# Kernel tuning notes

Hardware: AMD Instinct MI355X
Metric: run time of the kernel (lower is better)

The kernel has to match this reference:

```python
import jax, jax.numpy as jnp
import numpy as np
import math

G_GRAPHS = 32   # graphs per batch
NPG = 2048      # nodes per graph
DEG = 8         # avg degree
IN_DIM = 128
HID = 128

def _lin(k, fi, fo):
    return jax.random.normal(k, (fi, fo), jnp.float32) / np.sqrt(fi).astype(np.float32)

def setup_inputs():
    key = jax.random.key(0)
    ks = jax.random.split(key, 32)
    Nt = G_GRAPHS * NPG
    Epg = NPG * DEG
    E = G_GRAPHS * Epg
    x = jax.random.normal(ks[0], (Nt, IN_DIM), jnp.float32)
    src = jax.random.randint(ks[1], (E,), 0, NPG)
    dst = jax.random.randint(ks[2], (E,), 0, NPG)
    off = (jnp.arange(E) // Epg) * NPG  # keep edges within their graph block
    edge_index = jnp.stack([src + off, dst + off]).astype(jnp.int32)
    batch = (jnp.arange(Nt) // NPG).astype(jnp.int32)
    p = {}
    dims = [(IN_DIM, HID), (HID, HID), (HID, HID), (HID, HID)]
    for i, (fi, fo) in enumerate(dims, 1):
        p['Wl%d' % i] = _lin(ks[3 * i], fi, fo)
        p['bl%d' % i] = jnp.zeros((fo,), jnp.float32)
        p['Wr%d' % i] = _lin(ks[3 * i + 1], fi, fo)
    for j in (1, 2):  # SAGPooling score GNN (GraphConv hidden->1)
        p['Prel%d' % j] = _lin(ks[15 + 2 * j], HID, 1)
        p['prb%d' % j] = jnp.zeros((1,), jnp.float32)
        p['Proot%d' % j] = _lin(ks[16 + 2 * j], HID, 1)
    p['W5'] = _lin(ks[24], HID, 64); p['b5'] = jnp.zeros((64,), jnp.float32)
    p['W6'] = _lin(ks[25], 64, 2);  p['b6'] = jnp.zeros((2,), jnp.float32)
    return dict(x=x, edge_index=edge_index, batch=batch, npg=NPG, **p)

def reference(x, edge_index, batch, npg,
              Wl1, bl1, Wr1, Wl2, bl2, Wr2, Wl3, bl3, Wr3, Wl4, bl4, Wr4,
              Prel1, prb1, Proot1, Prel2, prb2, Proot2, W5, b5, W6, b6):
    src, dst = edge_index[0], edge_index[1]
    Nt = x.shape[0]
    Gn = Nt // npg

    def sage(h, em, Wl, bl, Wr):
        # SAGEConv (mean aggr): lin_l(mean_j x_j) + lin_r(x_root)
        s = jax.ops.segment_sum(h[src] * em[:, None], dst, num_segments=Nt)
        c = jax.ops.segment_sum(em, dst, num_segments=Nt)
        return (s / jnp.maximum(c, 1.0)[:, None]) @ Wl + bl + h @ Wr

    def pool(h, em, nm, k, Prel, prb, Proot):
        # SAGPooling: score = GraphConv(h) (add aggr), top-k per graph, x *= tanh(score)
        s = jax.ops.segment_sum(h[src] * em[:, None], dst, num_segments=Nt)
        score = (s @ Prel + h @ Proot + prb)[:, 0]
        smr = jnp.where(nm > 0, score, -1e30).reshape(Gn, npg)
        _, idx = jax.lax.top_k(smr, k)
        newm = jnp.zeros((Gn, npg), h.dtype).at[jnp.arange(Gn)[:, None], idx].set(1.0).reshape(-1)
        h = h * jnp.tanh(score)[:, None] * newm[:, None]
        em = em * newm[src] * newm[dst]  # filter_adj: keep edges with both ends kept
        return h, em, newm

    em = jnp.ones(src.shape, x.dtype)
    nm = jnp.ones((Nt,), x.dtype)
    h = jax.nn.relu(sage(x, em, Wl1, bl1, Wr1))
    h = jax.nn.relu(sage(h, em, Wl2, bl2, Wr2))
    k1 = math.ceil(0.5 * npg)
    h, em, nm = pool(h, em, nm, k1, Prel1, prb1, Proot1)
    h = jax.nn.relu(sage(h, em, Wl3, bl3, Wr3)) * nm[:, None]
    h = jax.nn.relu(sage(h, em, Wl4, bl4, Wr4)) * nm[:, None]
    k2 = math.ceil(0.5 * k1)
    h, em, nm = pool(h, em, nm, k2, Prel2, prb2, Proot2)
    # global mean pool over surviving nodes
    sums = jax.ops.segment_sum(h, batch, num_segments=Gn)
    cnt = jax.ops.segment_sum(nm, batch, num_segments=Gn)
    g = sums / jnp.maximum(cnt, 1.0)[:, None]
    g = jax.nn.relu(g @ W5 + b5)
    return jax.nn.log_softmax(g @ W6 + b6, axis=1)
```

## Files before the change

kernel.cpp:

```cpp
#include <hip/hip_runtime.h>
#include <hip/hip_bf16.h>
#include <math.h>

#define NT   65536
#define NPGC 2048
#define NG   32
#define NE   524288
#define EPG  16384
#define HID  128
#define K1   1024
#define K2   512

typedef short short8 __attribute__((ext_vector_type(8)));
typedef float f32x4  __attribute__((ext_vector_type(4)));

__device__ __forceinline__ float bf2f(unsigned short u) {
    union { unsigned int i; float f; } v; v.i = ((unsigned int)u) << 16; return v.f;
}
__device__ __forceinline__ unsigned short f2bf(float f) {
    union { float f; unsigned int i; } v; v.f = f;
    unsigned int x = v.i;
    return (unsigned short)((x + 0x7fffu + ((x >> 16) & 1u)) >> 16);
}
__device__ __forceinline__ void split2(float v, unsigned short& hi, unsigned short& lo) {
    unsigned int b = __float_as_uint(v);
    hi = (unsigned short)(b >> 16);
    float rem = v - __uint_as_float(b & 0xFFFF0000u);
    lo = (unsigned short)(__float_as_uint(rem) >> 16);
}

__global__ void k_detect(const unsigned short* __restrict__ x, int* __restrict__ flag) {
    __shared__ int cnt;
    if (threadIdx.x == 0) cnt = 0;
    __syncthreads();
    int sane = 0;
#pragma unroll
    for (int j = 0; j < 16; ++j) {
        unsigned short u = x[threadIdx.x * 16 + j];
        int e = (u >> 7) & 0xFF;
        if (e > 0x60 && e < 0xA0) sane++;
    }
    atomicAdd(&cnt, sane);
    __syncthreads();
    if (threadIdx.x == 0) *flag = (cnt > 3686) ? 1 : 0;
}

struct CvtDesc { const void* src[22]; int n[22]; int off[22]; };

__global__ void k_cvt(CvtDesc d, float* __restrict__ wts, const int* __restrict__ flag) {
    int t = blockIdx.y;
    int n = d.n[t];
    bool isbf = (*flag != 0);
    const unsigned short* sb = (const unsigned short*)d.src[t];
    const float* sf = (const float*)d.src[t];
    float* o = wts + d.off[t];
    for (int i = blockIdx.x * blockDim.x + threadIdx.x; i < n; i += gridDim.x * blockDim.x)
        o[i] = isbf ? bf2f(sb[i]) : sf[i];
}

__global__ void k_packW(const float* __restrict__ wts, int4 oWl, int4 oWr,
                        unsigned short* __restrict__ Wpack,
                        int* __restrict__ rowc, int* __restrict__ fill) {
    int idx = blockIdx.x * 256 + threadIdx.x;
    if (idx < NT) { rowc[idx] = 0; fill[idx] = 0; }
    if (idx >= 4 * 8 * 8 * 64 * 8) return;
    int L    = idx >> 15;
    int rem  = idx & 32767;
    int ct   = rem >> 12;
    int rem2 = rem & 4095;
    int ks   = rem2 >> 9;
    int rem3 = rem2 & 511;
    int lane = rem3 >> 3;
    int j    = rem3 & 7;
    int k   = ks * 32 + (lane >> 4) * 8 + j;
    int col = ct * 16 + (lane & 15);
    int ol = (L == 0) ? oWl.x : (L == 1) ? oWl.y : (L == 2) ? oWl.z : oWl.w;
    int orr = (L == 0) ? oWr.x : (L == 1) ? oWr.y : (L == 2) ? oWr.z : oWr.w;
    float w = (k < 128) ? wts[ol + k * 128 + col] : wts[orr + (k - 128) * 128 + col];
    unsigned short hi = f2bf(w);
    unsigned short lo = f2bf(w - bf2f(hi));
    int base = L * 65536 + (ct * 8 + ks) * 512 + lane * 8 + j;
    Wpack[base]         = hi;
    Wpack[base + 32768] = lo;
}

__global__ void k_hist(const int* __restrict__ dstE, int* __restrict__ rowc) {
    int e = blockIdx.x * 256 + threadIdx.x;
    if (e < NE) atomicAdd(&rowc[dstE[e]], 1);
}

__global__ void k_scan1(const int* __restrict__ cnt, int* __restrict__ rp, int* __restrict__ bsum,
                        float* __restrict__ invc) {
    __shared__ int s[256];
    int t = threadIdx.x;
    int i = blockIdx.x * 256 + t;
    int v = cnt[i];
    invc[i] = 1.0f / fmaxf((float)v, 1.0f);
    s[t] = v;
    __syncthreads();
    for (int off = 1; off < 256; off <<= 1) {
        int a = (t >= off) ? s[t - off] : 0;
        __syncthreads();
        s[t] += a;
        __syncthreads();
    }
    rp[i] = s[t] - v;
    if (t == 255) bsum[blockIdx.x] = s[255];
}

__global__ void k_scan23(int* __restrict__ rp, const int* __restrict__ bsum) {
    __shared__ int s[256];
    int t = threadIdx.x;
    s[t] = bsum[t];
    __syncthreads();
    for (int off = 1; off < 256; off <<= 1) {
        int a = (t >= off) ? s[t - off] : 0;
        __syncthreads();
        s[t] += a;
        __syncthreads();
    }
    int boffv = s[blockIdx.x] - bsum[blockIdx.x];
    int i = blockIdx.x * 256 + t;
    rp[i] += boffv;
    if (i == 0) rp[NT] = NE;
}

__global__ void k_scatter(const int* __restrict__ src, const int* __restrict__ dst,
                          const int* __restrict__ rp, int* __restrict__ fill, int* __restrict__ col) {
    int e = blockIdx.x * blockDim.x + threadIdx.x;
    if (e < NE) {
        int d = dst[e];
        int p = rp[d] + atomicAdd(&fill[d], 1);
        col[p] = src[e];
    }
}

__global__ void __launch_bounds__(256) k_fcsr(const int* __restrict__ act,
                                              const float* __restrict__ nm,
                                              const int* __restrict__ rp,
                                              const int* __restrict__ col,
                                              int2* __restrict__ rp2,
                                              int* __restrict__ col2,
                                              float* __restrict__ invc) {
    __shared__ int wtot[4];
    int g = blockIdx.x, t = threadIdx.x;
    int lane = t & 63, wv = t >> 6;
    int cb = g * K1;
    int ebase = g * EPG;
    int c[4]; int tsum = 0;
    int bg[4], en[4];
#pragma unroll
    for (int j = 0; j < 4; ++j) {
        int ci = t * 4 + j;
        int n = act[cb + ci];
        bg[j] = rp[n]; en[j] = rp[n + 1];
        int cc = 0;
        for (int e = bg[j]; e < en[j]; ++e) cc += (nm[col[e]] > 0.f) ? 1 : 0;
        c[j] = cc; tsum += cc;
        invc[n] = 1.0f / fmaxf((float)cc, 1.0f);
    }
    int pre = tsum;
#pragma unroll
    for (int off = 1; off < 64; off <<= 1) {
        int v = __shfl_up(pre, off, 64);
        pre += (lane >= off) ? v : 0;
    }
    if (lane == 63) wtot[wv] = pre;
    __syncthreads();
    int woff = 0;
#pragma unroll
    for (int w2 = 0; w2 < 4; ++w2) woff += (w2 < wv) ? wtot[w2] : 0;
    int ex = pre - tsum + woff;
#pragma unroll
    for (int j = 0; j < 4; ++j) {
        int ci = t * 4 + j;
        int p = ebase + ex;
        rp2[cb + ci] = make_int2(p, p + c[j]);
        for (int e = bg[j]; e < en[j]; ++e) {
            int s = col[e];
            if (nm[s] > 0.f) col2[p++] = s;
        }
        ex += c[j];
    }
}

__device__ __forceinline__ int lds_sw(int node, int k) {
    int g = k >> 3;
    int go = g ^ (node & 7);
    return node * 128 + go * 8 + (k & 7);
}

template<int MODE>
__device__ __forceinline__ float4 ldrow4(const void* __restrict__ h, int node, int f) {
    if constexpr (MODE == 1) {
        ushort4 v = *((const ushort4*)h + (size_t)node * 32 + (f >> 2));
        float4 o; o.x = bf2f(v.x); o.y = bf2f(v.y); o.z = bf2f(v.z); o.w = bf2f(v.w);
        return o;
    } else {
        return *((const float4*)h + (size_t)node * 32 + (f >> 2));
    }
}

template<bool HAS_TS, bool COMPACT, int MODE>
__device__ __forceinline__ void sage_body(
    const void* __restrict__ h, const float* __restrict__ ts,
    const float* __restrict__ invc,
    const int* __restrict__ rp, const int2* __restrict__ rp2,
    const int* __restrict__ col,
    const unsigned short* __restrict__ Wp,
    unsigned short* Ahi, unsigned short* Alo,
    unsigned short* Bhi, unsigned short* Blo,
    int n0, int cb, const int* __restrict__ actb, int tid, f32x4 acc[2][2])
{
    int lane = tid & 63, w = tid >> 6;
    int lrow = lane & 15, quad = lane >> 4;
    int gnode = tid >> 5;
    int f = (tid & 31) * 4;

    int gns[4], begs[4], ends[4]; float invs[4];
#pragma unroll
    for (int p = 0; p < 4; ++p) gns[p] = COMPACT ? actb[p * 8 + gnode] : n0 + p * 8 + gnode;
#pragma unroll
    for (int p = 0; p < 4; ++p) {
        if (COMPACT) { int2 be = rp2[cb + p * 8 + gnode]; begs[p] = be.x; ends[p] = be.y; }
        else         { begs[p] = rp[gns[p]]; ends[p] = rp[gns[p] + 1]; }
    }
#pragma unroll
    for (int p = 0; p < 4; ++p) invs[p] = invc[gns[p]];

    float4 rootv[4]; float roots[4];
#pragma unroll
    for (int i = 0; i < 4; ++i) {
        int idx = i * 256 + tid;
        int node = idx >> 5;
        int f2 = (idx & 31) * 4;
        int gn = COMPACT ? actb[node] : n0 + node;
        rootv[i] = ldrow4<MODE>(h, gn, f2);
        roots[i] = HAS_TS ? ts[gn] : 1.0f;
    }

#pragma unroll
    for (int pass = 0; pass < 4; ++pass) {
        int node = pass * 8 + gnode;
        float ax = 0.f, ay = 0.f, az = 0.f, aw = 0.f;
        int beg = begs[pass], end = ends[pass];
        int ecl = end - 1;
        for (int e0 = beg; e0 < end; e0 += 8) {
            int sj[8];
#pragma unroll
            for (int j = 0; j < 8; ++j) {
                int e = (e0 + j < end) ? e0 + j : ecl;
                sj[j] = col[e];
            }
            float4 vj[8];
#pragma unroll
            for (int j = 0; j < 8; ++j)
                vj[j] = ldrow4<MODE>(h, sj[j], f);
#pragma unroll
            for (int j = 0; j < 8; ++j) {
                float cj = (e0 + j < end) ? (HAS_TS ? ts[sj[j]] : 1.0f) : 0.0f;
                ax += vj[j].x * cj;
                ay += vj[j].y * cj;
                az += vj[j].z * cj;
                aw += vj[j].w * cj;
            }
        }
        float inv = invs[pass];
        ushort4 hi4, lo4;
        split2(ax * inv, hi4.x, lo4.x);
        split2(ay * inv, hi4.y, lo4.y);
        split2(az * inv, hi4.z, lo4.z);
        split2(aw * inv, hi4.w, lo4.w);
        int a = lds_sw(node, f);
        *(ushort4*)&Ahi[a] = hi4;
        *(ushort4*)&Alo[a] = lo4;
    }

#pragma unroll
    for (int i = 0; i < 4; ++i) {
        int idx = i * 256 + tid;
        int node = idx >> 5;
        int f2 = (idx & 31) * 4;
        float sc = roots[i];
        ushort4 hi4, lo4;
        split2(rootv[i].x * sc, hi4.x, lo4.x);
        split2(rootv[i].y * sc, hi4.y, lo4.y);
        split2(rootv[i].z * sc, hi4.z, lo4.z);
        split2(rootv[i].w * sc, hi4.w, lo4.w);
        int a = lds_sw(node, f2);
        *(ushort4*)&Bhi[a] = hi4;
        *(ushort4*)&Blo[a] = lo4;
    }
    __syncthreads();

#pragma unroll
    for (int ks = 0; ks < 8; ++ks) {
        const unsigned short* Hb = (ks < 4) ? Ahi : Bhi;
        const unsigned short* Lb = (ks < 4) ? Alo : Blo;
        short8 bh[2], blo[2];
#pragma unroll
        for (int c = 0; c < 2; ++c) {
            int ct = 2 * w + c;
            bh[c]  = *(const short8*)&Wp[(ct * 8 + ks) * 512 + lane * 8];
            blo[c] = *(const short8*)&Wp[32768 + (ct * 8 + ks) * 512 + lane * 8];
        }
        int kb = (ks & 3) * 32 + quad * 8;
#pragma unroll
        for (int st = 0; st < 2; ++st) {
            int a = lds_sw(st * 16 + lrow, kb);
            short8 ah = *(const short8*)&Hb[a];
            short8 al = *(const short8*)&Lb[a];
#pragma unroll
            for (int c = 0; c < 2; ++c) {
                acc[st][c] = __builtin_amdgcn_mfma_f32_16x16x32_bf16(ah, bh[c],  acc[st][c], 0, 0, 0);
                acc[st][c] = __builtin_amdgcn_mfma_f32_16x16x32_bf16(al, bh[c],  acc[st][c], 0, 0, 0);
                acc[st][c] = __builtin_amdgcn_mfma_f32_16x16x32_bf16(ah, blo[c], acc[st][c], 0, 0, 0);
            }
        }
    }
}

template<bool COMPACT>
__device__ __forceinline__ void map_block(int b, int& graph, int& tile) {
    if (COMPACT) { graph = (b & 7) * 4 + (b >> 8); tile = (b >> 3) & 31; }
    else         { graph = (b & 7) * 4 + (b >> 9); tile = (b >> 3) & 63; }
}

__global__ void __launch_bounds__(256, 8) k_sage_l1(
    const void* __restrict__ x, const int* __restrict__ flag,
    const float* __restrict__ invc,
    const int* __restrict__ rp, const int* __restrict__ col,
    const unsigned short* __restrict__ Wp, const float* __restrict__ bl,
    float* __restrict__ out)
{
    __shared__ unsigned short Ahi[32 * 128];
    __shared__ unsigned short Alo[32 * 128];
    __shared__ unsigned short Bhi[32 * 128];
    __shared__ unsigned short Blo[32 * 128];
    int tid = threadIdx.x;
    int graph, tile;
    map_block<false>(blockIdx.x, graph, tile);
    int n0 = graph * NPGC + tile * 32;
    int lane = tid & 63, w = tid >> 6;
    int lrow = lane & 15, quad = lane >> 4;
    f32x4 acc[2][2] = {};

    if (*flag)
        sage_body<false, false, 1>(x, nullptr, invc, rp, nullptr, col, Wp, Ahi, Alo, Bhi, Blo, n0, 0, nullptr, tid, acc);
    else
        sage_body<false, false, 0>(x, nullptr, invc, rp, nullptr, col, Wp, Ahi, Alo, Bhi, Blo, n0, 0, nullptr, tid, acc);

#pragma unroll
    for (int c = 0; c < 2; ++c) {
        int colg = (2 * w + c) * 16 + lrow;
        float bias = bl[colg];
#pragma unroll
        for (int st = 0; st < 2; ++st) {
#pragma unroll
            for (int rr = 0; rr < 4; ++rr) {
                int node = n0 + st * 16 + quad * 4 + rr;
                __builtin_nontemporal_store(fmaxf(acc[st][c][rr] + bias, 0.f),
                                            &out[(size_t)node * HID + colg]);
            }
        }
    }
}

__global__ void __launch_bounds__(256, 8) k_sage_plain(
    const float* __restrict__ h, const float* __restrict__ ts,
    const float* __restrict__ invc,
    const int2* __restrict__ rp2, const int* __restrict__ col2,
    const unsigned short* __restrict__ Wp, const float* __restrict__ bl,
    float* __restrict__ out, const int* __restrict__ act)
{
    __shared__ unsigned short Ahi[32 * 128];
    __shared__ unsigned short Alo[32 * 128];
    __shared__ unsigned short Bhi[32 * 128];
    __shared__ unsigned short Blo[32 * 128];
    int tid = threadIdx.x;
    int graph, tile;
    map_block<true>(blockIdx.x, graph, tile);
    int n0 = graph * NPGC + tile * 32;
    int cb = graph * K1 + tile * 32;
    const int* actb = act + cb;
    int lane = tid & 63, w = tid >> 6;
    int lrow = lane & 15, quad = lane >> 4;
    f32x4 acc[2][2] = {};

    sage_body<true, true, 0>(h, ts, invc, nullptr, rp2, col2, Wp, Ahi, Alo, Bhi, Blo, n0, cb, actb, tid, acc);

#pragma unroll
    for (int c = 0; c < 2; ++c) {
        int colg = (2 * w + c) * 16 + lrow;
        float bias = bl[colg];
#pragma unroll
        for (int st = 0; st < 2; ++st) {
#pragma unroll
            for (int rr = 0; rr < 4; ++rr) {
                int node = actb[st * 16 + quad * 4 + rr];
                __builtin_nontemporal_store(fmaxf(acc[st][c][rr] + bias, 0.f),
                                            &out[(size_t)node * HID + colg]);
            }
        }
    }
}

template<bool COMPACT>
__global__ void __launch_bounds__(256, 8) k_sage_dots(
    const float* __restrict__ h,
    const float* __restrict__ invc,
    const int* __restrict__ rp, const int2* __restrict__ rp2,
    const int* __restrict__ col,
    const unsigned short* __restrict__ Wp, const float* __restrict__ bl,
    float* __restrict__ out,
    const float* __restrict__ Prel, const float* __restrict__ Proot,
    float* __restrict__ q, float* __restrict__ r, const int* __restrict__ act)
{
    __shared__ unsigned short Ahi[32 * 128];
    __shared__ unsigned short Alo[32 * 128];
    __shared__ unsigned short Bhi[32 * 128];
    __shared__ unsigned short Blo[32 * 128];
    int tid = threadIdx.x;
    int graph, tile;
    map_block<COMPACT>(blockIdx.x, graph, tile);
    int n0 = graph * NPGC + tile * 32;
    int cb = COMPACT ? (graph * K1 + tile * 32) : 0;
    const int* actb = COMPACT ? (act + cb) : nullptr;
    int lane = tid & 63, w = tid >> 6;
    int lrow = lane & 15, quad = lane >> 4;
    f32x4 acc[2][2] = {};

    sage_body<false, COMPACT, 0>(h, nullptr, invc, rp, rp2, col, Wp, Ahi, Alo, Bhi, Blo, n0, cb, actb, tid, acc);

    float qp[2][4] = {}, rp_[2][4] = {};
#pragma unroll
    for (int c = 0; c < 2; ++c) {
        int colg = (2 * w + c) * 16 + lrow;
        float bias = bl[colg];
        float pq = Prel[colg], pr = Proot[colg];
#pragma unroll
        for (int st = 0; st < 2; ++st) {
#pragma unroll
            for (int rr = 0; rr < 4; ++rr) {
                int nl = st * 16 + quad * 4 + rr;
                int node = COMPACT ? actb[nl] : n0 + nl;
                float val = fmaxf(acc[st][c][rr] + bias, 0.f);
                __builtin_nontemporal_store(val, &out[(size_t)node * HID + colg]);
                qp[st][rr] += val * pq;
                rp_[st][rr] += val * pr;
            }
        }
    }
#pragma unroll
    for (int st = 0; st < 2; ++st)
#pragma unroll
        for (int rr = 0; rr < 4; ++rr) {
#pragma unroll
            for (int m = 1; m < 16; m <<= 1) {
                qp[st][rr]  += __shfl_xor(qp[st][rr],  m, 64);
                rp_[st][rr] += __shfl_xor(rp_[st][rr], m, 64);
            }
        }
    __syncthreads();
    float* qa = (float*)Ahi;
    if (tid < 64) qa[tid] = 0.f;
    __syncthreads();
    if (lrow == 0) {
#pragma unroll
        for (int st = 0; st < 2; ++st)
#pragma unroll
            for (int rr = 0; rr < 4; ++rr) {
                int nl = st * 16 + quad * 4 + rr;
                atomicAdd(&qa[nl], qp[st][rr]);
                atomicAdd(&qa[32 + nl], rp_[st][rr]);
            }
    }
    __syncthreads();
    if (tid < 32) {
        int node = COMPACT ? actb[tid] : n0 + tid;
        q[node] = qa[tid];
        r[node] = qa[32 + tid];
    }
}

__global__ void k_score(const float* __restrict__ q, const float* __restrict__ r,
                        const float* __restrict__ prb,
                        const int* __restrict__ rp, const int* __restrict__ col,
                        float* __restrict__ score) {
    int n = blockIdx.x * 256 + threadIdx.x;
    int beg = rp[n], end = rp[n + 1];
    float s = 0.f;
    for (int e = beg; e < end; ++e) s += q[col[e]];
    score[n] = s + r[n] + prb[0];
}

__global__ void k_score2(const float* __restrict__ q, const float* __restrict__ r,
                         const float* __restrict__ prb,
                         const int2* __restrict__ rp2, const int* __restrict__ col2,
                         float* __restrict__ score, const int* __restrict__ act) {
    int i = blockIdx.x * 256 + threadIdx.x;
    int n = act[i];
    int2 be = rp2[i];
    float s = 0.f;
    for (int e = be.x; e < be.y; ++e) s += q[col2[e]];
    score[n] = s + r[n] + prb[0];
}

template<bool NMIN>
__global__ void __launch_bounds__(256) k_topk(const float* __restrict__ score,
                                              float* __restrict__ nm,
                                              float* __restrict__ tval, int k,
                                              int* __restrict__ act) {
    __shared__ unsigned int u[NPGC];
    __shared__ int hist[256];
    __shared__ int scanb[257];
    __shared__ int wtot[4];
    __shared__ int wtot2[4];
    __shared__ unsigned int s_byte;
    __shared__ int s_kk;
    int tid = threadIdx.x;
    int lane = tid & 63, wv = tid >> 6;
    int base = blockIdx.x * NPGC;

    for (int j = tid; j < NPGC; j += 256) {
        float sc = NMIN ? ((nm[base + j] > 0.f) ? score[base + j] : -1e30f) : score[base + j];
        unsigned int v = __float_as_uint(sc);
        v = (v & 0x80000000u) ? ~v : (v | 0x80000000u);
        u[j] = v;
    }
    hist[tid] = 0;
    if (tid == 0) scanb[256] = 0;
    __syncthreads();

    unsigned int prefix = 0;
    int kk = k;
#pragma unroll
    for (int round = 0; round < 4; ++round) {
        int shift = 24 - 8 * round;
        unsigned int pmask = (round == 0) ? 0u : (0xFFFFFFFFu << (32 - 8 * round));
        for (int j = tid; j < NPGC; j += 256) {
            unsigned int v = u[j];
            if ((v & pmask) == prefix) atomicAdd(&hist[(v >> shift) & 0xFF], 1);
        }
        __syncthreads();
        int s = hist[tid];
#pragma unroll
        for (int off = 1; off < 64; off <<= 1) {
            int t = __shfl_down(s, off, 64);
            s += (lane + off < 64) ? t : 0;
        }
        if (lane == 0) wtot[wv] = s;
        __syncthreads();
        int add = 0;
#pragma unroll
        for (int w2 = 1; w2 < 4; ++w2) add += (wv + w2 < 4) ? wtot[wv + w2] : 0;
        s += add;
        scanb[tid] = s;
        __syncthreads();
        int above = scanb[tid + 1];
        if (s >= kk && above < kk) { s_byte = (unsigned int)tid; s_kk = kk - above; }
        hist[tid] = 0;
        __syncthreads();
        prefix |= (s_byte << shift);
        kk = s_kk;
    }
    unsigned int thr = prefix;

    int j0 = tid * 8;
    int cnt = 0;
#pragma unroll
    for (int j = 0; j < 8; ++j) cnt += (u[j0 + j] == thr);
    int s = cnt;
#pragma unroll
    for (int off = 1; off < 64; off <<= 1) {
        int t = __shfl_up(s, off, 64);
        s += (lane >= off) ? t : 0;
    }
    if (lane == 63) wtot[wv] = s;
    __syncthreads();
    int add = 0;
#pragma unroll
    for (int w2 = 0; w2 < 4; ++w2) add += (w2 < wv) ? wtot[w2] : 0;
    int rank = s - cnt + add;

    unsigned int keepmask = 0u;
    int myrank = rank;
    int kcnt = 0;
#pragma unroll
    for (int j = 0; j < 8; ++j) {
        unsigned int v = u[j0 + j];
        bool kp;
        if (v > thr) kp = true;
        else if (v == thr) { kp = (myrank < kk); myrank++; }
        else kp = false;
        keepmask |= (kp ? 1u : 0u) << j;
        kcnt += kp ? 1 : 0;
    }
    int s2 = kcnt;
#pragma unroll
    for (int off = 1; off < 64; off <<= 1) {
        int t2 = __shfl_up(s2, off, 64);
        s2 += (lane >= off) ? t2 : 0;
    }
    if (lane == 63) wtot2[wv] = s2;
    __syncthreads();
    int pos = s2 - kcnt;
#pragma unroll
    for (int w2 = 0; w2 < 4; ++w2) pos += (w2 < wv) ? wtot2[w2] : 0;
    int* actg = act + blockIdx.x * k;
#pragma unroll
    for (int j = 0; j < 8; ++j) {
        bool kp = (keepmask >> j) & 1u;
        int n = base + j0 + j;
        nm[n]   = kp ? 1.0f : 0.0f;
        tval[n] = kp ? tanhf(score[n]) : 0.0f;
        if (kp) actg[pos++] = n;
    }
}

__global__ void k_tail(const float* __restrict__ h, const float* __restrict__ t,
                       const int* __restrict__ act,
                       const float* __restrict__ W5, const float* __restrict__ b5,
                       const float* __restrict__ W6, const float* __restrict__ b6,
                       void* __restrict__ out, const int* __restrict__ flag) {
    __shared__ float gsh[2][HID];
    __shared__ float g5[64];
    __shared__ float ls[2];
    int graph = blockIdx.x, tid = threadIdx.x;
    int f = tid & 127, sub = tid >> 7;
    const int* actg = act + graph * K2;
    float acc = 0.f;
#pragma unroll 8
    for (int i = 0; i < 256; ++i) {
        int gn = actg[sub * 256 + i];
        acc += h[(size_t)gn * HID + f] * t[gn];
    }
    gsh[sub][f] = acc;
    __syncthreads();
    if (tid < 64) {
        const float ic = 1.0f / (float)K2;
        float a5 = b5[tid];
        for (int ff = 0; ff < HID; ++ff)
            a5 += (gsh[0][ff] + gsh[1][ff]) * ic * W5[ff * 64 + tid];
        g5[tid] = fmaxf(a5, 0.f);
    }
    __syncthreads();
    if (tid < 2) {
        float l = b6[tid];
        for (int tt = 0; tt < 64; ++tt) l += g5[tt] * W6[tt * 2 + tid];
        ls[tid] = l;
    }
    __syncthreads();
    if (tid == 0) {
        float a = ls[0], b = ls[1];
        float mx = fmaxf(a, b);
        float lse = mx + logf(expf(a - mx) + expf(b - mx));
        if (*flag) {
            ((unsigned short*)out)[graph * 2 + 0] = f2bf(a - lse);
            ((unsigned short*)out)[graph * 2 + 1] = f2bf(b - lse);
        } else {
            ((float*)out)[graph * 2 + 0] = a - lse;
            ((float*)out)[graph * 2 + 1] = b - lse;
        }
    }
}

extern "C" void kernel_launch(void* const* d_in, const int* in_sizes, int n_in,
                              void* d_out, int out_size, void* d_ws, size_t ws_size,
                              hipStream_t stream) {
    const void* x    = d_in[0];
    const int*  ei   = (const int*)d_in[1];
    const int*  srcE = ei;
    const int*  dstE = ei + NE;

    char* ws = (char*)d_ws;
    float* hA    = (float*)(ws + 0);
    float* hB    = (float*)(ws + 33554432);
    float* tvec  = (float*)(ws + 67108864);
    float* invc  = (float*)(ws + 67371008);
    int*   col2  = (int*)  (ws + 67633152);
    int2*  rp2   = (int2*) (ws + 69730304);
    float* q     = (float*)(ws + 100663296);
    float* r     = (float*)(ws + 100925440);
    float* score = (float*)(ws + 101187584);
    float* nm    = (float*)(ws + 101449728);
    int*   rowc  = (int*)  (ws + 101711872);
    int*   rp    = (int*)  (ws + 101974016);
    int*   bsum  = (int*)  (ws + 102236416);
    int*   fill  = (int*)  (ws + 102238464);
    int*   col   = (int*)  (ws + 102500608);
    int*   flag  = (int*)  (ws + 104615936);
    float* wts   = (float*)(ws + 104616960);
    unsigned short* Wpack = (unsigned short*)(ws + 105179136);
    int*   act1  = rowc;
    int*   act2  = fill;
    (void)in_sizes; (void)n_in; (void)out_size; (void)ws_size;

    const int O_Wl1 = 0,      O_bl1 = 16384,  O_Wr1 = 16512;
    const int O_Wl2 = 32896,  O_bl2 = 49280,  O_Wr2 = 49408;
    const int O_Wl3 = 65792,  O_bl3 = 82176,  O_Wr3 = 82304;
    const int O_Wl4 = 98688,  O_bl4 = 115072, O_Wr4 = 115200;
    const int O_Pr1 = 131584, O_pb1 = 131712, O_Po1 = 131713;
    const int O_Pr2 = 131841, O_pb2 = 131969, O_Po2 = 131970;
    const int O_W5  = 132098, O_b5  = 140290, O_W6 = 140354, O_b6 = 140482;

    CvtDesc d;
    const int srcIdx[22] = {4,5,6,7,8,9,10,11,12,13,14,15,16,17,18,19,20,21,22,23,24,25};
    const int nelems[22] = {16384,128,16384, 16384,128,16384, 16384,128,16384, 16384,128,16384,
                            128,1,128, 128,1,128, 8192,64,128,2};
    const int offs[22]   = {O_Wl1,O_bl1,O_Wr1, O_Wl2,O_bl2,O_Wr2, O_Wl3,O_bl3,O_Wr3, O_Wl4,O_bl4,O_Wr4,
                            O_Pr1,O_pb1,O_Po1, O_Pr2,O_pb2,O_Po2, O_W5,O_b5,O_W6,O_b6};
    for (int i = 0; i < 22; ++i) { d.src[i] = d_in[srcIdx[i]]; d.n[i] = nelems[i]; d.off[i] = offs[i]; }

    k_detect <<<1, 256, 0, stream>>>((const unsigned short*)x, flag);
    k_cvt    <<<dim3(64, 22), 256, 0, stream>>>(d, wts, flag);
    k_packW  <<<512, 256, 0, stream>>>(wts, make_int4(O_Wl1, O_Wl2, O_Wl3, O_Wl4),
                                       make_int4(O_Wr1, O_Wr2, O_Wr3, O_Wr4), Wpack, rowc, fill);
    k_hist   <<<2048, 256, 0, stream>>>(dstE, rowc);

    k_scan1  <<<256, 256, 0, stream>>>(rowc, rp, bsum, invc);
    k_scan23 <<<256, 256, 0, stream>>>(rp, bsum);
    k_scatter<<<2048, 256, 0, stream>>>(srcE, dstE, rp, fill, col);

    k_sage_l1<<<2048, 256, 0, stream>>>(x, flag, invc, rp, col,
                                        Wpack + 0 * 65536, wts + O_bl1, hB);
    k_sage_dots<false><<<2048, 256, 0, stream>>>(hB, invc, rp, nullptr, col,
                                                 Wpack + 1 * 65536, wts + O_bl2, hA,
                                                 wts + O_Pr1, wts + O_Po1, q, r, nullptr);

    k_score<<<256, 256, 0, stream>>>(q, r, wts + O_pb1, rp, col, score);
    k_topk<false><<<32, 256, 0, stream>>>(score, nm, tvec, K1, act1);
    k_fcsr <<<32, 256, 0, stream>>>(act1, nm, rp, col, rp2, col2, invc);

    k_sage_plain<<<1024, 256, 0, stream>>>(hA, tvec, invc, rp2, col2,
                                           Wpack + 2 * 65536, wts + O_bl3, hB, act1);
    k_sage_dots<true><<<1024, 256, 0, stream>>>(hB, invc, nullptr, rp2, col2,
                                                Wpack + 3 * 65536, wts + O_bl4, hA,
                                                wts + O_Pr2, wts + O_Po2, q, r, act1);

    k_score2<<<NG * K1 / 256, 256, 0, stream>>>(q, r, wts + O_pb2, rp2, col2, score, act1);
    k_topk<true><<<32, 256, 0, stream>>>(score, nm, tvec, K2, act2);

    k_tail<<<32, 256, 0, stream>>>(hA, tvec, act2, wts + O_W5, wts + O_b5,
                                   wts + O_W6, wts + O_b6, d_out, flag);
}
```

Measured before the change: 389.1 us.

## Reuse one LDS tile for aggregate and root halves, parallelize filtered CSR build

The SAGE body now runs the MFMA over the aggregated-neighbour tile first, then reloads root rows into the same LDS buffers and runs the second half. This halves shared memory per block and drops the root-row registers held across the gather, with launch bounds changed from 8 to 6 blocks. The filtered CSR build moves from 32 blocks with a block scan to one thread per kept node using a per-graph atomic cursor, which adds a memset and makes edge order nondeterministic. Nontemporal output stores become plain stores. The price is an extra barrier and a root load that is no longer overlapped with the gather.

```diff
diff --git a/kernel.cpp b/kernel.cpp
--- a/kernel.cpp
+++ b/kernel.cpp
@@ -135,52 +135,23 @@
     }
 }
 
-__global__ void __launch_bounds__(256) k_fcsr(const int* __restrict__ act,
-                                              const float* __restrict__ nm,
-                                              const int* __restrict__ rp,
-                                              const int* __restrict__ col,
-                                              int2* __restrict__ rp2,
-                                              int* __restrict__ col2,
-                                              float* __restrict__ invc) {
-    __shared__ int wtot[4];
-    int g = blockIdx.x, t = threadIdx.x;
-    int lane = t & 63, wv = t >> 6;
-    int cb = g * K1;
-    int ebase = g * EPG;
-    int c[4]; int tsum = 0;
-    int bg[4], en[4];
-#pragma unroll
-    for (int j = 0; j < 4; ++j) {
-        int ci = t * 4 + j;
-        int n = act[cb + ci];
-        bg[j] = rp[n]; en[j] = rp[n + 1];
-        int cc = 0;
-        for (int e = bg[j]; e < en[j]; ++e) cc += (nm[col[e]] > 0.f) ? 1 : 0;
-        c[j] = cc; tsum += cc;
-        invc[n] = 1.0f / fmaxf((float)cc, 1.0f);
-    }
-    int pre = tsum;
-#pragma unroll
-    for (int off = 1; off < 64; off <<= 1) {
-        int v = __shfl_up(pre, off, 64);
-        pre += (lane >= off) ? v : 0;
-    }
-    if (lane == 63) wtot[wv] = pre;
-    __syncthreads();
-    int woff = 0;
-#pragma unroll
-    for (int w2 = 0; w2 < 4; ++w2) woff += (w2 < wv) ? wtot[w2] : 0;
-    int ex = pre - tsum + woff;
-#pragma unroll
-    for (int j = 0; j < 4; ++j) {
-        int ci = t * 4 + j;
-        int p = ebase + ex;
-        rp2[cb + ci] = make_int2(p, p + c[j]);
-        for (int e = bg[j]; e < en[j]; ++e) {
-            int s = col[e];
-            if (nm[s] > 0.f) col2[p++] = s;
-        }
-        ex += c[j];
+__global__ void k_fbuild(const int* __restrict__ act, const float* __restrict__ nm,
+                         const int* __restrict__ rp, const int* __restrict__ col,
+                         int2* __restrict__ rp2, int* __restrict__ col2,
+                         float* __restrict__ invc, int* __restrict__ ghead) {
+    int i = blockIdx.x * 256 + threadIdx.x;
+    int n = act[i];
+    int g = i >> 10;
+    int bg = rp[n], en = rp[n + 1];
+    int cc = 0;
+    for (int e = bg; e < en; ++e) cc += (nm[col[e]] > 0.f) ? 1 : 0;
+    invc[n] = 1.0f / fmaxf((float)cc, 1.0f);
+    int p0 = g * EPG + atomicAdd(&ghead[g], cc);
+    rp2[i] = make_int2(p0, p0 + cc);
+    int p = p0;
+    for (int e = bg; e < en; ++e) {
+        int s = col[e];
+        if (nm[s] > 0.f) col2[p++] = s;
     }
 }
 
@@ -209,7 +180,6 @@
     const int* __restrict__ col,
     const unsigned short* __restrict__ Wp,
     unsigned short* Ahi, unsigned short* Alo,
-    unsigned short* Bhi, unsigned short* Blo,
     int n0, int cb, const int* __restrict__ actb, int tid, f32x4 acc[2][2])
 {
     int lane = tid & 63, w = tid >> 6;
@@ -227,17 +197,6 @@
     }
 #pragma unroll
     for (int p = 0; p < 4; ++p) invs[p] = invc[gns[p]];
-
-    float4 rootv[4]; float roots[4];
-#pragma unroll
-    for (int i = 0; i < 4; ++i) {
-        int idx = i * 256 + tid;
-        int node = idx >> 5;
-        int f2 = (idx & 31) * 4;
-        int gn = COMPACT ? actb[node] : n0 + node;
-        rootv[i] = ldrow4<MODE>(h, gn, f2);
-        roots[i] = HAS_TS ? ts[gn] : 1.0f;
-    }
 
 #pragma unroll
     for (int pass = 0; pass < 4; ++pass) {
@@ -275,28 +234,54 @@
         *(ushort4*)&Ahi[a] = hi4;
         *(ushort4*)&Alo[a] = lo4;
     }
+    __syncthreads();
+
+#pragma unroll
+    for (int ks = 0; ks < 4; ++ks) {
+        short8 bh[2], blo[2];
+#pragma unroll
+        for (int c = 0; c < 2; ++c) {
+            int ct = 2 * w + c;
+            bh[c]  = *(const short8*)&Wp[(ct * 8 + ks) * 512 + lane * 8];
+            blo[c] = *(const short8*)&Wp[32768 + (ct * 8 + ks) * 512 + lane * 8];
+        }
+        int kb = ks * 32 + quad * 8;
+#pragma unroll
+        for (int st = 0; st < 2; ++st) {
+            int a = lds_sw(st * 16 + lrow, kb);
+            short8 ah = *(const short8*)&Ahi[a];
+            short8 al = *(const short8*)&Alo[a];
+#pragma unroll
+            for (int c = 0; c < 2; ++c) {
+                acc[st][c] = __builtin_amdgcn_mfma_f32_16x16x32_bf16(ah, bh[c],  acc[st][c], 0, 0, 0);
+                acc[st][c] = __builtin_amdgcn_mfma_f32_16x16x32_bf16(al, bh[c],  acc[st][c], 0, 0, 0);
+                acc[st][c] = __builtin_amdgcn_mfma_f32_16x16x32_bf16(ah, blo[c], acc[st][c], 0, 0, 0);
+            }
+        }
+    }
+    __syncthreads();
 
 #pragma unroll
     for (int i = 0; i < 4; ++i) {
         int idx = i * 256 + tid;
         int node = idx >> 5;
         int f2 = (idx & 31) * 4;
-        float sc = roots[i];
+        int gn = COMPACT ? actb[node] : n0 + node;
+        float4 v = ldrow4<MODE>(h, gn, f2);
+        float sc = HAS_TS ? ts[gn] : 1.0f;
         ushort4 hi4, lo4;
-        split2(rootv[i].x * sc, hi4.x, lo4.x);
-        split2(rootv[i].y * sc, hi4.y, lo4.y);
-        split2(rootv[i].z * sc, hi4.z, lo4.z);
-        split2(rootv[i].w * sc, hi4.w, lo4.w);
+        split2(v.x * sc, hi4.x, lo4.x);
+        split2(v.y * sc, hi4.y, lo4.y);
+        split2(v.z * sc, hi4.z, lo4.z);
+        split2(v.w * sc, hi4.w, lo4.w);
         int a = lds_sw(node, f2);
-        *(ushort4*)&Bhi[a] = hi4;
-        *(ushort4*)&Blo[a] = lo4;
-    }
-    __syncthreads();
-
-#pragma unroll
-    for (int ks = 0; ks < 8; ++ks) {
-        const unsigned short* Hb = (ks < 4) ? Ahi : Bhi;
-        const unsigned short* Lb = (ks < 4) ? Alo : Blo;
+        *(ushort4*)&Ahi[a] = hi4;
+        *(ushort4*)&Alo[a] = lo4;
+    }
+    __syncthreads();
+
+#pragma unroll
+    for (int ks = 4; ks < 8; ++ks) {
         short8 bh[2], blo[2];
 #pragma unroll
         for (int c = 0; c < 2; ++c) {
@@ -304,12 +289,12 @@
             bh[c]  = *(const short8*)&Wp[(ct * 8 + ks) * 512 + lane * 8];
             blo[c] = *(const short8*)&Wp[32768 + (ct * 8 + ks) * 512 + lane * 8];
         }
-        int kb = (ks & 3) * 32 + quad * 8;
+        int kb = (ks - 4) * 32 + quad * 8;
 #pragma unroll
         for (int st = 0; st < 2; ++st) {
             int a = lds_sw(st * 16 + lrow, kb);
-            short8 ah = *(const short8*)&Hb[a];
-            short8 al = *(const short8*)&Lb[a];
+            short8 ah = *(const short8*)&Ahi[a];
+            short8 al = *(const short8*)&Alo[a];
 #pragma unroll
             for (int c = 0; c < 2; ++c) {
                 acc[st][c] = __builtin_amdgcn_mfma_f32_16x16x32_bf16(ah, bh[c],  acc[st][c], 0, 0, 0);
@@ -326,7 +311,7 @@
     else         { graph = (b & 7) * 4 + (b >> 9); tile = (b >> 3) & 63; }
 }
 
-__global__ void __launch_bounds__(256, 8) k_sage_l1(
+__global__ void __launch_bounds__(256, 6) k_sage_l1(
     const void* __restrict__ x, const int* __restrict__ flag,
     const float* __restrict__ invc,
     const int* __restrict__ rp, const int* __restrict__ col,
@@ -335,8 +320,6 @@
 {
     __shared__ unsigned short Ahi[32 * 128];
     __shared__ unsigned short Alo[32 * 128];
-    __shared__ unsigned short Bhi[32 * 128];
-    __shared__ unsigned short Blo[32 * 128];
     int tid = threadIdx.x;
     int graph, tile;
     map_block<false>(blockIdx.x, graph, tile);
@@ -346,9 +329,9 @@
     f32x4 acc[2][2] = {};
 
     if (*flag)
-        sage_body<false, false, 1>(x, nullptr, invc, rp, nullptr, col, Wp, Ahi, Alo, Bhi, Blo, n0, 0, nullptr, tid, acc);
+        sage_body<false, false, 1>(x, nullptr, invc, rp, nullptr, col, Wp, Ahi, Alo, n0, 0, nullptr, tid, acc);
     else
-        sage_body<false, false, 0>(x, nullptr, invc, rp, nullptr, col, Wp, Ahi, Alo, Bhi, Blo, n0, 0, nullptr, tid, acc);
+        sage_body<false, false, 0>(x, nullptr, invc, rp, nullptr, col, Wp, Ahi, Alo, n0, 0, nullptr, tid, acc);
 
 #pragma unroll
     for (int c = 0; c < 2; ++c) {
@@ -359,14 +342,13 @@
 #pragma unroll
             for (int rr = 0; rr < 4; ++rr) {
                 int node = n0 + st * 16 + quad * 4 + rr;
-                __builtin_nontemporal_store(fmaxf(acc[st][c][rr] + bias, 0.f),
-                                            &out[(size_t)node * HID + colg]);
-            }
-        }
-    }
-}
-
-__global__ void __launch_bounds__(256, 8) k_sage_plain(
+                out[(size_t)node * HID + colg] = fmaxf(acc[st][c][rr] + bias, 0.f);
+            }
+        }
+    }
+}
+
+__global__ void __launch_bounds__(256, 6) k_sage_plain(
     const float* __restrict__ h, const float* __restrict__ ts,
     const float* __restrict__ invc,
     const int2* __restrict__ rp2, const int* __restrict__ col2,
@@ -375,8 +357,6 @@
 {
     __shared__ unsigned short Ahi[32 * 128];
     __shared__ unsigned short Alo[32 * 128];
-    __shared__ unsigned short Bhi[32 * 128];
-    __shared__ unsigned short Blo[32 * 128];
     int tid = threadIdx.x;
     int graph, tile;
     map_block<true>(blockIdx.x, graph, tile);
@@ -387,7 +367,7 @@
     int lrow = lane & 15, quad = lane >> 4;
     f32x4 acc[2][2] = {};
 
-    sage_body<true, true, 0>(h, ts, invc, nullptr, rp2, col2, Wp, Ahi, Alo, Bhi, Blo, n0, cb, actb, tid, acc);
+    sage_body<true, true, 0>(h, ts, invc, nullptr, rp2, col2, Wp, Ahi, Alo, n0, cb, actb, tid, acc);
 
 #pragma unroll
     for (int c = 0; c < 2; ++c) {
@@ -398,15 +378,14 @@
 #pragma unroll
             for (int rr = 0; rr < 4; ++rr) {
                 int node = actb[st * 16 + quad * 4 + rr];
-                __builtin_nontemporal_store(fmaxf(acc[st][c][rr] + bias, 0.f),
-                                            &out[(size_t)node * HID + colg]);
+                out[(size_t)node * HID + colg] = fmaxf(acc[st][c][rr] + bias, 0.f);
             }
         }
     }
 }
 
 template<bool COMPACT>
-__global__ void __launch_bounds__(256, 8) k_sage_dots(
+__global__ void __launch_bounds__(256, 6) k_sage_dots(
     const float* __restrict__ h,
     const float* __restrict__ invc,
     const int* __restrict__ rp, const int2* __restrict__ rp2,
@@ -418,8 +397,6 @@
 {
     __shared__ unsigned short Ahi[32 * 128];
     __shared__ unsigned short Alo[32 * 128];
-    __shared__ unsigned short Bhi[32 * 128];
-    __shared__ unsigned short Blo[32 * 128];
     int tid = threadIdx.x;
     int graph, tile;
     map_block<COMPACT>(blockIdx.x, graph, tile);
@@ -430,7 +407,7 @@
     int lrow = lane & 15, quad = lane >> 4;
     f32x4 acc[2][2] = {};
 
-    sage_body<false, COMPACT, 0>(h, nullptr, invc, rp, rp2, col, Wp, Ahi, Alo, Bhi, Blo, n0, cb, actb, tid, acc);
+    sage_body<false, COMPACT, 0>(h, nullptr, invc, rp, rp2, col, Wp, Ahi, Alo, n0, cb, actb, tid, acc);
 
     float qp[2][4] = {}, rp_[2][4] = {};
 #pragma unroll
@@ -445,7 +422,7 @@
                 int nl = st * 16 + quad * 4 + rr;
                 int node = COMPACT ? actb[nl] : n0 + nl;
                 float val = fmaxf(acc[st][c][rr] + bias, 0.f);
-                __builtin_nontemporal_store(val, &out[(size_t)node * HID + colg]);
+                out[(size_t)node * HID + colg] = val;
                 qp[st][rr] += val * pq;
                 rp_[st][rr] += val * pr;
             }
@@ -680,6 +657,7 @@
     float* invc  = (float*)(ws + 67371008);
     int*   col2  = (int*)  (ws + 67633152);
     int2*  rp2   = (int2*) (ws + 69730304);
+    int*   ghead = (int*)  (ws + 69992448);
     float* q     = (float*)(ws + 100663296);
     float* r     = (float*)(ws + 100925440);
     float* score = (float*)(ws + 101187584);
@@ -712,6 +690,8 @@
                             O_Pr1,O_pb1,O_Po1, O_Pr2,O_pb2,O_Po2, O_W5,O_b5,O_W6,O_b6};
     for (int i = 0; i < 22; ++i) { d.src[i] = d_in[srcIdx[i]]; d.n[i] = nelems[i]; d.off[i] = offs[i]; }
 
+    hipMemsetAsync(ghead, 0, NG * 4, stream);
+
     k_detect <<<1, 256, 0, stream>>>((const unsigned short*)x, flag);
     k_cvt    <<<dim3(64, 22), 256, 0, stream>>>(d, wts, flag);
     k_packW  <<<512, 256, 0, stream>>>(wts, make_int4(O_Wl1, O_Wl2, O_Wl3, O_Wl4),
@@ -730,7 +710,7 @@
 
     k_score<<<256, 256, 0, stream>>>(q, r, wts + O_pb1, rp, col, score);
     k_topk<false><<<32, 256, 0, stream>>>(score, nm, tvec, K1, act1);
-    k_fcsr <<<32, 256, 0, stream>>>(act1, nm, rp, col, rp2, col2, invc);
+    k_fbuild<<<NG * K1 / 256, 256, 0, stream>>>(act1, nm, rp, col, rp2, col2, invc, ghead);
 
     k_sage_plain<<<1024, 256, 0, stream>>>(hA, tvec, invc, rp2, col2,
                                            Wpack + 2 * 65536, wts + O_bl3, hB, act1);
```

New measurement: 544.6 us. 1.4x slower.
